# Kernel tuning notes

Measured on AMD Instinct MI355X. Metric: run time of the kernel, lower is better.

The kernel has to match this reference:

```python
import jax, jax.numpy as jnp
import numpy as np

OUT_DIM = 65536
G = 2            # num_global_crops
L = 8            # num_local_crops
T = G + L        # num_total_crops
B = 64           # batch_size
STUDENT_TEMP = 0.1
TEACHER_TEMP = 0.04
CENTER_MOMENTUM = 0.9


def setup_inputs() -> dict:
    key = jax.random.key(0)
    k1, k2 = jax.random.split(key)
    student_output = jax.random.normal(k1, (B * T, OUT_DIM), dtype=jnp.float32)
    teacher_output = jax.random.normal(k2, (B * G, OUT_DIM), dtype=jnp.float32)
    center = jnp.zeros((1, OUT_DIM), dtype=jnp.float32)
    return {
        "student_output": student_output,
        "teacher_output": teacher_output,
        "center": center,
        "batch_size": B,
        "epoch": 0,
    }


def reference(student_output, teacher_output, center, batch_size, epoch):
    # Teacher temperature schedule: epoch < warmup_epochs(=0) never true -> teacher_temp
    teacher_temp = TEACHER_TEMP

    # (B, T, D) scaled student logits
    s = (student_output / STUDENT_TEMP).reshape(batch_size, T, -1)
    # (B, G, D) teacher softmax probabilities
    t_probs = jax.nn.softmax(teacher_output / teacher_temp, axis=-1).reshape(batch_size, G, -1)

    # Center update (buffer is updated BEFORE being used, matching the torch code)
    batch_center = jnp.mean(t_probs.reshape(-1, t_probs.shape[-1]), axis=0, keepdims=True)  # (1, D)
    new_center = center * CENTER_MOMENTUM + batch_center * (1.0 - CENTER_MOMENTUM)
    t_centered = t_probs - new_center  # broadcast (1,D) over (B,G,D)

    # Stable log-softmax over student crops: (B, T, D)
    logp = jax.nn.log_softmax(s, axis=-1)

    # Cross terms for all (teacher crop g, student crop t) pairs, summed over batch:
    # cross[b, g, t] = -sum_d t_centered[b,g,d] * logp[b,t,d]
    cross = -jnp.einsum("bgd,btd->bgt", t_centered, logp)  # (B, G, T)

    # Skip same-view pairs (s_idx == t_idx and s_idx < G), i.e. diagonal of the GxG block
    mask = jnp.ones((G, T), dtype=cross.dtype).at[jnp.arange(G), jnp.arange(G)].set(0.0)
    total_loss = jnp.sum(cross * mask)

    n_loss_terms = batch_size * G * (T - 1)
    return jnp.reshape(total_loss / n_loss_terms, (1,))
```

## Files before the change

### kernel.cpp

```cpp
#include <hip/hip_runtime.h>
#include <math.h>

#define NC_OFF    4096
#define SE_OFF    1024
#define SP_OFF    16
#define COEF0_OFF 131072
#define COEF1_OFF 4325376
#define COMB_OFF  8519680

constexpr float INV_ST = 10.0f;
constexpr float INV_TT = 25.0f;
constexpr float CS = 64.0f;
constexpr float CT = 100.0f;

__device__ __forceinline__ float wave_sum(float v) {
#pragma unroll
    for (int off = 32; off > 0; off >>= 1) v += __shfl_down(v, off, 64);
    return v;
}

__device__ __forceinline__ float block_sum_256(float v) {
    __shared__ float ls[4];
    v = wave_sum(v);
    int lane = threadIdx.x & 63, wv = threadIdx.x >> 6;
    if (lane == 0) ls[wv] = v;
    __syncthreads();
    return ls[0] + ls[1] + ls[2] + ls[3];
}

__global__ void k0_zero(float* __restrict__ ws) {
    int tid = threadIdx.x;
#pragma unroll
    for (int i = 0; i < 8; ++i) ws[tid + i * 256] = 0.0f;
}

__global__ void __launch_bounds__(256) k1_rowsum(
        const float* __restrict__ te, float* __restrict__ ws) {
    int bid = blockIdx.x;
    int r = bid >> 2, ch = bid & 3;
    const float4* p = (const float4*)te + (size_t)r * 16384 + ch * 4096;
    int tid = threadIdx.x;
    float se = 0.0f;
#pragma unroll 4
    for (int i = 0; i < 16; ++i) {
        float4 v = p[tid + (i << 8)];
        se += __expf(fmaf(v.x, INV_TT, -CT));
        se += __expf(fmaf(v.y, INV_TT, -CT));
        se += __expf(fmaf(v.z, INV_TT, -CT));
        se += __expf(fmaf(v.w, INV_TT, -CT));
    }
    se = block_sum_256(se);
    if (threadIdx.x == 0) ws[SP_OFF + bid] = se;
}

__global__ void __launch_bounds__(256) k2_nc(
        const float* __restrict__ te, const float* __restrict__ center,
        float* __restrict__ ws) {
    __shared__ float rS[128];
    int tid = threadIdx.x;
    if (tid < 128) {
        float s = ws[SP_OFF + tid * 4] + ws[SP_OFF + tid * 4 + 1]
                + ws[SP_OFF + tid * 4 + 2] + ws[SP_OFF + tid * 4 + 3];
        rS[tid] = 1.0f / s;
    }
    __syncthreads();
    int d = blockIdx.x * 256 + tid;
    float a = 0.0f;
#pragma unroll 8
    for (int r = 0; r < 128; ++r) {
        float u = te[((size_t)r << 16) + d];
        a += __expf(fmaf(u, INV_TT, -CT)) * rS[r];
    }
    float ncv = fmaf(0.9f, center[d], a * (1.0f / 1280.0f));
    ws[NC_OFF + d] = ncv;
    float s = block_sum_256(ncv);
    if (tid == 0) atomicAdd(&ws[0], s);
}

__global__ void __launch_bounds__(256) k2c_coef(
        const float* __restrict__ te, float* __restrict__ ws) {
    int bid = blockIdx.x;
    int b = bid >> 2, ch = bid & 3;
    int ra = 2 * b, rb = 2 * b + 1;
    float sa = ws[SP_OFF + ra * 4] + ws[SP_OFF + ra * 4 + 1]
             + ws[SP_OFF + ra * 4 + 2] + ws[SP_OFF + ra * 4 + 3];
    float sb = ws[SP_OFF + rb * 4] + ws[SP_OFF + rb * 4 + 1]
             + ws[SP_OFF + rb * 4 + 2] + ws[SP_OFF + rb * 4 + 3];
    float rsa = 1.0f / sa, rsb = 1.0f / sb;

    int tid = threadIdx.x;
    int cbase = ch * 4096 + tid;
    const float4* ta = (const float4*)te + (size_t)ra * 16384 + cbase;
    const float4* tb = (const float4*)te + (size_t)rb * 16384 + cbase;
    const float4* nc = (const float4*)(ws + NC_OFF) + cbase;
    float4* c0 = (float4*)(ws + COEF0_OFF) + (size_t)b * 16384 + cbase;
    float4* c1 = (float4*)(ws + COEF1_OFF) + (size_t)b * 16384 + cbase;
    float4* cc = (float4*)(ws + COMB_OFF) + (size_t)b * 16384 + cbase;

#pragma unroll 2
    for (int i = 0; i < 16; ++i) {
        int idx = i << 8;
        float4 av = ta[idx], bv = tb[idx], nv = nc[idx];
        float4 v0, v1, vc;
        float pa, pb;
        pa = __expf(fmaf(av.x, INV_TT, -CT)) * rsa; pb = __expf(fmaf(bv.x, INV_TT, -CT)) * rsb;
        v0.x = nv.x - pb; v1.x = nv.x - pa; vc.x = v0.x + v1.x;
        pa = __expf(fmaf(av.y, INV_TT, -CT)) * rsa; pb = __expf(fmaf(bv.y, INV_TT, -CT)) * rsb;
        v0.y = nv.y - pb; v1.y = nv.y - pa; vc.y = v0.y + v1.y;
        pa = __expf(fmaf(av.z, INV_TT, -CT)) * rsa; pb = __expf(fmaf(bv.z, INV_TT, -CT)) * rsb;
        v0.z = nv.z - pb; v1.z = nv.z - pa; vc.z = v0.z + v1.z;
        pa = __expf(fmaf(av.w, INV_TT, -CT)) * rsa; pb = __expf(fmaf(bv.w, INV_TT, -CT)) * rsb;
        v0.w = nv.w - pb; v1.w = nv.w - pa; vc.w = v0.w + v1.w;
        c0[idx] = v0; c1[idx] = v1; cc[idx] = vc;
    }
}

__global__ void __launch_bounds__(256) k3_student(
        const float* __restrict__ st, float* __restrict__ ws) {
    int bid = blockIdx.x;
    int row = bid >> 1, half = bid & 1;
    int b = row / 10, t = row - b * 10;
    const float* coef_base =
        (t == 0) ? (ws + COEF0_OFF) : ((t == 1) ? (ws + COEF1_OFF) : (ws + COMB_OFF));

    int tid = threadIdx.x;
    size_t fbase = (size_t)half * 8192 + tid;
    const float4* xr = (const float4*)st + (size_t)row * 16384 + fbase;
    const float4* cf = (const float4*)coef_base + (size_t)b * 16384 + fbase;

    float dot = 0.0f, se = 0.0f;
#pragma unroll 4
    for (int i = 0; i < 32; ++i) {
        int idx = i << 8;
        float4 xv = xr[idx];
        float4 cv = cf[idx];
        float s0 = xv.x * INV_ST, s1 = xv.y * INV_ST, s2 = xv.z * INV_ST, s3 = xv.w * INV_ST;
        dot = fmaf(cv.x, s0, dot); se += __expf(s0 - CS);
        dot = fmaf(cv.y, s1, dot); se += __expf(s1 - CS);
        dot = fmaf(cv.z, s2, dot); se += __expf(s2 - CS);
        dot = fmaf(cv.w, s3, dot); se += __expf(s3 - CS);
    }
    dot = wave_sum(dot);
    se = wave_sum(se);
    __shared__ float ld[4], lss[4];
    int lane = tid & 63, wv = tid >> 6;
    if (lane == 0) { ld[wv] = dot; lss[wv] = se; }
    __syncthreads();
    if (tid == 0) {
        atomicAdd(&ws[1], ld[0] + ld[1] + ld[2] + ld[3]);
        atomicAdd(&ws[SE_OFF + row], lss[0] + lss[1] + lss[2] + lss[3]);
    }
}

__global__ void __launch_bounds__(640) k4_final(
        const float* __restrict__ ws, float* __restrict__ out) {
    int tid = threadIdx.x;
    int t = tid % 10;
    float w = (t < 2) ? 1.0f : 2.0f;
    float Z = CS + __logf(ws[SE_OFF + tid]);
    float v = w * Z;
    v = wave_sum(v);
    __shared__ float ls[10];
    int lane = tid & 63, wv = tid >> 6;
    if (lane == 0) ls[wv] = v;
    __syncthreads();
    if (tid == 0) {
        float zs = 0.0f;
#pragma unroll
        for (int i = 0; i < 10; ++i) zs += ls[i];
        out[0] = (ws[1] + (1.0f - ws[0]) * zs) * (1.0f / 1152.0f);
    }
}

extern "C" void kernel_launch(void* const* d_in, const int* in_sizes, int n_in,
                              void* d_out, int out_size, void* d_ws, size_t ws_size,
                              hipStream_t stream) {
    const float* st = (const float*)d_in[0];
    const float* te = (const float*)d_in[1];
    const float* center = (const float*)d_in[2];
    float* ws = (float*)d_ws;
    float* out = (float*)d_out;

    hipLaunchKernelGGL(k0_zero, dim3(1), dim3(256), 0, stream, ws);
    hipLaunchKernelGGL(k1_rowsum, dim3(512), dim3(256), 0, stream, te, ws);
    hipLaunchKernelGGL(k2_nc, dim3(256), dim3(256), 0, stream, te, center, ws);
    hipLaunchKernelGGL(k2c_coef, dim3(256), dim3(256), 0, stream, te, ws);
    hipLaunchKernelGGL(k3_student, dim3(1280), dim3(256), 0, stream, st, ws);
    hipLaunchKernelGGL(k4_final, dim3(1), dim3(640), 0, stream, ws, out);
}
```

Before: 290.7 us.

## Fuse teacher coefficient computation into student pass, drop coef buffers and zero kernel

Teacher-centered coefficients are now built in registers inside the student kernel instead of being written to a roughly 100 MB workspace and read back. Each block keeps its coefficients and reuses them across all ten crops of a batch item. This removes the large coefficient write and read traffic and two launches. Zeroing of the accumulators moves into the first kernel, and the dot accumulator becomes per-batch slots summed in the final kernel. In exchange there are many more per-wave atomics, and the teacher rows are re-read and exponentials recomputed.

After: 285.0 us. 2.0% less time.

```diff
diff --git a/kernel.cpp b/kernel.cpp
--- a/kernel.cpp
+++ b/kernel.cpp
@@ -1,12 +1,10 @@
 #include <hip/hip_runtime.h>
 #include <math.h>
 
-#define NC_OFF    4096
-#define SE_OFF    1024
-#define SP_OFF    16
-#define COEF0_OFF 131072
-#define COEF1_OFF 4325376
-#define COMB_OFF  8519680
+#define SE_OFF  16
+#define DOT_OFF 704
+#define SP_OFF  1024
+#define NC_OFF  2048
 
 constexpr float INV_ST = 10.0f;
 constexpr float INV_TT = 25.0f;
@@ -19,27 +17,13 @@
     return v;
 }
 
-__device__ __forceinline__ float block_sum_256(float v) {
-    __shared__ float ls[4];
-    v = wave_sum(v);
-    int lane = threadIdx.x & 63, wv = threadIdx.x >> 6;
-    if (lane == 0) ls[wv] = v;
-    __syncthreads();
-    return ls[0] + ls[1] + ls[2] + ls[3];
-}
-
-__global__ void k0_zero(float* __restrict__ ws) {
-    int tid = threadIdx.x;
-#pragma unroll
-    for (int i = 0; i < 8; ++i) ws[tid + i * 256] = 0.0f;
-}
-
 __global__ void __launch_bounds__(256) k1_rowsum(
         const float* __restrict__ te, float* __restrict__ ws) {
     int bid = blockIdx.x;
+    int tid = threadIdx.x;
+    if (bid < 384 && tid < 2) ws[bid * 2 + tid] = 0.0f;
     int r = bid >> 2, ch = bid & 3;
     const float4* p = (const float4*)te + (size_t)r * 16384 + ch * 4096;
-    int tid = threadIdx.x;
     float se = 0.0f;
 #pragma unroll 4
     for (int i = 0; i < 16; ++i) {
@@ -49,8 +33,12 @@
         se += __expf(fmaf(v.z, INV_TT, -CT));
         se += __expf(fmaf(v.w, INV_TT, -CT));
     }
-    se = block_sum_256(se);
-    if (threadIdx.x == 0) ws[SP_OFF + bid] = se;
+    se = wave_sum(se);
+    __shared__ float ls[4];
+    int lane = tid & 63, wv = tid >> 6;
+    if (lane == 0) ls[wv] = se;
+    __syncthreads();
+    if (tid == 0) ws[SP_OFF + bid] = ls[0] + ls[1] + ls[2] + ls[3];
 }
 
 __global__ void __launch_bounds__(256) k2_nc(
@@ -73,83 +61,81 @@
     }
     float ncv = fmaf(0.9f, center[d], a * (1.0f / 1280.0f));
     ws[NC_OFF + d] = ncv;
-    float s = block_sum_256(ncv);
-    if (tid == 0) atomicAdd(&ws[0], s);
+    float s = wave_sum(ncv);
+    __shared__ float ls[4];
+    int lane = tid & 63, wv = tid >> 6;
+    if (lane == 0) ls[wv] = s;
+    __syncthreads();
+    if (tid == 0) atomicAdd(&ws[0], ls[0] + ls[1] + ls[2] + ls[3]);
 }
 
-__global__ void __launch_bounds__(256) k2c_coef(
-        const float* __restrict__ te, float* __restrict__ ws) {
+__global__ void __launch_bounds__(256) k3_fused(
+        const float* __restrict__ st, const float* __restrict__ te,
+        float* __restrict__ ws) {
     int bid = blockIdx.x;
-    int b = bid >> 2, ch = bid & 3;
-    int ra = 2 * b, rb = 2 * b + 1;
-    float sa = ws[SP_OFF + ra * 4] + ws[SP_OFF + ra * 4 + 1]
+    int b = bid >> 4, ch = bid & 15;
+    int ra = 2 * b, rb = ra + 1;
+    float Sa = ws[SP_OFF + ra * 4] + ws[SP_OFF + ra * 4 + 1]
              + ws[SP_OFF + ra * 4 + 2] + ws[SP_OFF + ra * 4 + 3];
-    float sb = ws[SP_OFF + rb * 4] + ws[SP_OFF + rb * 4 + 1]
+    float Sb = ws[SP_OFF + rb * 4] + ws[SP_OFF + rb * 4 + 1]
              + ws[SP_OFF + rb * 4 + 2] + ws[SP_OFF + rb * 4 + 3];
-    float rsa = 1.0f / sa, rsb = 1.0f / sb;
+    float rsa = 1.0f / Sa, rsb = 1.0f / Sb;
 
     int tid = threadIdx.x;
-    int cbase = ch * 4096 + tid;
-    const float4* ta = (const float4*)te + (size_t)ra * 16384 + cbase;
-    const float4* tb = (const float4*)te + (size_t)rb * 16384 + cbase;
-    const float4* nc = (const float4*)(ws + NC_OFF) + cbase;
-    float4* c0 = (float4*)(ws + COEF0_OFF) + (size_t)b * 16384 + cbase;
-    float4* c1 = (float4*)(ws + COEF1_OFF) + (size_t)b * 16384 + cbase;
-    float4* cc = (float4*)(ws + COMB_OFF) + (size_t)b * 16384 + cbase;
+    size_t fbase = (size_t)ch * 1024 + tid;
+    const float4* ta = (const float4*)te + (size_t)ra * 16384 + fbase;
+    const float4* tb = (const float4*)te + (size_t)rb * 16384 + fbase;
+    const float4* nc = (const float4*)(ws + NC_OFF) + fbase;
 
-#pragma unroll 2
-    for (int i = 0; i < 16; ++i) {
-        int idx = i << 8;
-        float4 av = ta[idx], bv = tb[idx], nv = nc[idx];
-        float4 v0, v1, vc;
+    float4 c0[4], c1[4], cL[4];
+#pragma unroll
+    for (int k = 0; k < 4; ++k) {
+        float4 av = ta[k * 256], bv = tb[k * 256], nv = nc[k * 256];
         float pa, pb;
-        pa = __expf(fmaf(av.x, INV_TT, -CT)) * rsa; pb = __expf(fmaf(bv.x, INV_TT, -CT)) * rsb;
-        v0.x = nv.x - pb; v1.x = nv.x - pa; vc.x = v0.x + v1.x;
-        pa = __expf(fmaf(av.y, INV_TT, -CT)) * rsa; pb = __expf(fmaf(bv.y, INV_TT, -CT)) * rsb;
-        v0.y = nv.y - pb; v1.y = nv.y - pa; vc.y = v0.y + v1.y;
-        pa = __expf(fmaf(av.z, INV_TT, -CT)) * rsa; pb = __expf(fmaf(bv.z, INV_TT, -CT)) * rsb;
-        v0.z = nv.z - pb; v1.z = nv.z - pa; vc.z = v0.z + v1.z;
-        pa = __expf(fmaf(av.w, INV_TT, -CT)) * rsa; pb = __expf(fmaf(bv.w, INV_TT, -CT)) * rsb;
-        v0.w = nv.w - pb; v1.w = nv.w - pa; vc.w = v0.w + v1.w;
-        c0[idx] = v0; c1[idx] = v1; cc[idx] = vc;
+        pa = __expf(fmaf(av.x, INV_TT, -CT)) * rsa;
+        pb = __expf(fmaf(bv.x, INV_TT, -CT)) * rsb;
+        c0[k].x = (nv.x - pb) * INV_ST; c1[k].x = (nv.x - pa) * INV_ST;
+        cL[k].x = c0[k].x + c1[k].x;
+        pa = __expf(fmaf(av.y, INV_TT, -CT)) * rsa;
+        pb = __expf(fmaf(bv.y, INV_TT, -CT)) * rsb;
+        c0[k].y = (nv.y - pb) * INV_ST; c1[k].y = (nv.y - pa) * INV_ST;
+        cL[k].y = c0[k].y + c1[k].y;
+        pa = __expf(fmaf(av.z, INV_TT, -CT)) * rsa;
+        pb = __expf(fmaf(bv.z, INV_TT, -CT)) * rsb;
+        c0[k].z = (nv.z - pb) * INV_ST; c1[k].z = (nv.z - pa) * INV_ST;
+        cL[k].z = c0[k].z + c1[k].z;
+        pa = __expf(fmaf(av.w, INV_TT, -CT)) * rsa;
+        pb = __expf(fmaf(bv.w, INV_TT, -CT)) * rsb;
+        c0[k].w = (nv.w - pb) * INV_ST; c1[k].w = (nv.w - pa) * INV_ST;
+        cL[k].w = c0[k].w + c1[k].w;
     }
-}
 
-__global__ void __launch_bounds__(256) k3_student(
-        const float* __restrict__ st, float* __restrict__ ws) {
-    int bid = blockIdx.x;
-    int row = bid >> 1, half = bid & 1;
-    int b = row / 10, t = row - b * 10;
-    const float* coef_base =
-        (t == 0) ? (ws + COEF0_OFF) : ((t == 1) ? (ws + COEF1_OFF) : (ws + COMB_OFF));
+    const float4* xbase = (const float4*)st + (size_t)(b * 10) * 16384 + fbase;
+    int lane = tid & 63;
+    float q = 0.0f;
 
-    int tid = threadIdx.x;
-    size_t fbase = (size_t)half * 8192 + tid;
-    const float4* xr = (const float4*)st + (size_t)row * 16384 + fbase;
-    const float4* cf = (const float4*)coef_base + (size_t)b * 16384 + fbase;
+    auto do_row = [&](int t, const float4* cf) {
+        const float4* xr = xbase + (size_t)t * 16384;
+        float se = 0.0f;
+#pragma unroll
+        for (int k = 0; k < 4; ++k) {
+            float4 xv = xr[k * 256];
+            q = fmaf(cf[k].x, xv.x, q); se += __expf(fmaf(xv.x, INV_ST, -CS));
+            q = fmaf(cf[k].y, xv.y, q); se += __expf(fmaf(xv.y, INV_ST, -CS));
+            q = fmaf(cf[k].z, xv.z, q); se += __expf(fmaf(xv.z, INV_ST, -CS));
+            q = fmaf(cf[k].w, xv.w, q); se += __expf(fmaf(xv.w, INV_ST, -CS));
+        }
+        se = wave_sum(se);
+        if (lane == 0) atomicAdd(&ws[SE_OFF + b * 10 + t], se);
+    };
 
-    float dot = 0.0f, se = 0.0f;
-#pragma unroll 4
-    for (int i = 0; i < 32; ++i) {
-        int idx = i << 8;
-        float4 xv = xr[idx];
-        float4 cv = cf[idx];
-        float s0 = xv.x * INV_ST, s1 = xv.y * INV_ST, s2 = xv.z * INV_ST, s3 = xv.w * INV_ST;
-        dot = fmaf(cv.x, s0, dot); se += __expf(s0 - CS);
-        dot = fmaf(cv.y, s1, dot); se += __expf(s1 - CS);
-        dot = fmaf(cv.z, s2, dot); se += __expf(s2 - CS);
-        dot = fmaf(cv.w, s3, dot); se += __expf(s3 - CS);
-    }
-    dot = wave_sum(dot);
-    se = wave_sum(se);
-    __shared__ float ld[4], lss[4];
-    int lane = tid & 63, wv = tid >> 6;
-    if (lane == 0) { ld[wv] = dot; lss[wv] = se; }
-    __syncthreads();
-    if (tid == 0) {
-        atomicAdd(&ws[1], ld[0] + ld[1] + ld[2] + ld[3]);
-        atomicAdd(&ws[SE_OFF + row], lss[0] + lss[1] + lss[2] + lss[3]);
-    }
+    do_row(0, c0);
+    do_row(1, c1);
+#pragma unroll
+    for (int t = 2; t < 10; ++t) do_row(t, cL);
+
+    q = wave_sum(q);
+    if (lane == 0) atomicAdd(&ws[DOT_OFF + b], q);
 }
 
 __global__ void __launch_bounds__(640) k4_final(
@@ -157,18 +143,19 @@
     int tid = threadIdx.x;
     int t = tid % 10;
     float w = (t < 2) ? 1.0f : 2.0f;
-    float Z = CS + __logf(ws[SE_OFF + tid]);
-    float v = w * Z;
-    v = wave_sum(v);
-    __shared__ float ls[10];
+    float zv = w * (CS + __logf(ws[SE_OFF + tid]));
+    float dv = (tid < 64) ? ws[DOT_OFF + tid] : 0.0f;
+    zv = wave_sum(zv);
+    dv = wave_sum(dv);
+    __shared__ float lz[10], ldt[10];
     int lane = tid & 63, wv = tid >> 6;
-    if (lane == 0) ls[wv] = v;
+    if (lane == 0) { lz[wv] = zv; ldt[wv] = dv; }
     __syncthreads();
     if (tid == 0) {
-        float zs = 0.0f;
+        float zs = 0.0f, ds = 0.0f;
 #pragma unroll
-        for (int i = 0; i < 10; ++i) zs += ls[i];
-        out[0] = (ws[1] + (1.0f - ws[0]) * zs) * (1.0f / 1152.0f);
+        for (int i = 0; i < 10; ++i) { zs += lz[i]; ds += ldt[i]; }
+        out[0] = (ds + (1.0f - ws[0]) * zs) * (1.0f / 1152.0f);
     }
 }
 
@@ -181,10 +168,8 @@
     float* ws = (float*)d_ws;
     float* out = (float*)d_out;
 
-    hipLaunchKernelGGL(k0_zero, dim3(1), dim3(256), 0, stream, ws);
     hipLaunchKernelGGL(k1_rowsum, dim3(512), dim3(256), 0, stream, te, ws);
     hipLaunchKernelGGL(k2_nc, dim3(256), dim3(256), 0, stream, te, center, ws);
-    hipLaunchKernelGGL(k2c_coef, dim3(256), dim3(256), 0, stream, te, ws);
-    hipLaunchKernelGGL(k3_student, dim3(1280), dim3(256), 0, stream, st, ws);
+    hipLaunchKernelGGL(k3_fused, dim3(1024), dim3(256), 0, stream, st, te, ws);
     hipLaunchKernelGGL(k4_final, dim3(1), dim3(640), 0, stream, ws, out);
 }
```
